# Performance work log

Hardware: AMD Instinct MI355X
Metric: run time of the kernel (lower is better)

## Reference

```python
import jax, jax.numpy as jnp
import numpy as np

ALPHA_LO = float(np.exp(-1.0 / 5.0))   # 0.8187
ALPHA_HI = float(np.exp(-1.0 / 25.0))  # 0.9608
BN_EPS = 1e-5

B, T, D_IN, H = 32, 2000, 512, 512


def setup_inputs() -> dict:
    key = jax.random.key(0)
    ks = jax.random.split(key, 5)
    x = jax.random.normal(ks[0], (B, T, D_IN), dtype=jnp.float32)
    W = jax.random.normal(ks[1], (H, D_IN), dtype=jnp.float32) / np.sqrt(D_IN)
    b = jax.random.normal(ks[2], (H,), dtype=jnp.float32) * 0.01
    alpha = jax.random.uniform(ks[3], (H,), dtype=jnp.float32,
                               minval=ALPHA_LO, maxval=ALPHA_HI)
    gamma = jnp.ones((H,), dtype=jnp.float32)
    beta = jnp.zeros((H,), dtype=jnp.float32)
    ut0 = jax.random.uniform(ks[4], (B, H), dtype=jnp.float32)
    return {"x": x, "W": W, "b": b, "alpha": alpha,
            "gamma": gamma, "beta": beta, "ut0": ut0}


def reference(x, W, b, alpha, gamma, beta, ut0):
    # Linear: [B,T,Din] @ [Din,H] + b
    Wx = jnp.einsum("btd,hd->bth", x, W) + b
    # BatchNorm1d (training forward): stats over flattened (B*T) dim
    flat = Wx.reshape(-1, Wx.shape[-1])
    mean = flat.mean(axis=0)
    var = flat.var(axis=0)  # biased, as torch BN uses for normalization
    Wx = ((flat - mean) * jax.lax.rsqrt(var + BN_EPS) * gamma + beta).reshape(Wx.shape)
    # Readout cell: leaky integration + softmax accumulation over time
    a = jnp.clip(alpha, ALPHA_LO, ALPHA_HI)

    def step(carry, wxt):
        ut, acc = carry
        ut = a * ut + (1.0 - a) * wxt          # [B,H]
        acc = acc + jax.nn.softmax(ut, axis=1)
        return (ut, acc), None

    wx_t = jnp.transpose(Wx, (1, 0, 2))  # [T,B,H]
    (_, out), _ = jax.lax.scan(step, (ut0, jnp.zeros_like(ut0)), wx_t)
    return out[:, None, :]  # [B,1,H]
```

## Files before the change

### kernel.cpp

```cpp
#include <hip/hip_runtime.h>
#include <hip/hip_bf16.h>
#include <stdint.h>


namespace {
constexpr int kB = 32;
constexpr int kT = 2000;
constexpr int kD = 512;
constexpr int kH = 512;
constexpr int kM = kB * kT;
constexpr int kL = 20;
constexpr int kC = kT / kL;
constexpr float kALo = 0.81873075307798182f;
constexpr float kAHi = 0.96078943915232320f;

typedef __bf16 bf16x4 __attribute__((ext_vector_type(4)));
typedef __bf16 bf16x8 __attribute__((ext_vector_type(8)));
typedef float floatx16 __attribute__((ext_vector_type(16)));

__device__ __forceinline__ float bf2f(unsigned short u) {
  return __builtin_bit_cast(float, (unsigned)u << 16);
}
__device__ __forceinline__ float clipa(float a) {
  return fminf(fmaxf(a, kALo), kAHi);
}
__device__ __forceinline__ float pow20(float a) {
  const float a2 = a * a, a4 = a2 * a2, a5 = a4 * a;
  const float a10 = a5 * a5;
  return a10 * a10;
}
__device__ __forceinline__ void gld_lds16(const void* g, void* l) {
  __builtin_amdgcn_global_load_lds(
      (const __attribute__((address_space(1))) uint32_t*)g,
      (__attribute__((address_space(3))) uint32_t*)(uintptr_t)l, 16, 0, 0);
}

__global__ __launch_bounds__(256) void wcvt_k(const float* __restrict__ W,
                                              __bf16* __restrict__ Wbf) {
  const int t = blockIdx.x * 256 + threadIdx.x;
  const float4 a0 = ((const float4*)W)[t * 2];
  const float4 a1 = ((const float4*)W)[t * 2 + 1];
  bf16x8 v;
  v[0] = (__bf16)a0.x; v[1] = (__bf16)a0.y; v[2] = (__bf16)a0.z; v[3] = (__bf16)a0.w;
  v[4] = (__bf16)a1.x; v[5] = (__bf16)a1.y; v[6] = (__bf16)a1.z; v[7] = (__bf16)a1.w;
  *(bf16x8*)(Wbf + (size_t)t * 8) = v;
}

__global__ __launch_bounds__(512, 2) void gemm_k(const float* __restrict__ X,
                                                 const __bf16* __restrict__ Wbf,
                                                 unsigned short* __restrict__ Wxb,
                                                 float* __restrict__ partial) {
  __shared__ __bf16 As[64][32];
  __shared__ __bf16 Bs[512][32];
  __shared__ float sred[2][kH];
  const int tid = threadIdx.x;
  const size_t row0 = (size_t)blockIdx.x * 64;
  const int w = tid >> 6, L = tid & 63;
  const int rt = w >> 2, ct0 = (w & 3) * 4;
  const int lhalf = L >> 5, l32 = L & 31;
  const int arow = tid >> 3, acol = (tid & 7) * 4;

  floatx16 acc[4] = {};
  const float* xbase = X + (row0 + arow) * kD + acol;
  float4 a_pre = *(const float4*)xbase;

#pragma unroll 1
  for (int s = 0; s < 16; ++s) {
    __syncthreads();
    bf16x4 av;
    av[0] = (__bf16)a_pre.x; av[1] = (__bf16)a_pre.y;
    av[2] = (__bf16)a_pre.z; av[3] = (__bf16)a_pre.w;
    *(bf16x4*)&As[arow][acol] = av;
    const int kk = s * 32;
#pragma unroll
    for (int j = 0; j < 4; ++j) {
      const int ci = j * 512 + w * 64 + L;
      const __bf16* src = Wbf + (size_t)(ci >> 2) * kD + kk + (ci & 3) * 8;
      gld_lds16(src, (char*)&Bs[0][0] + (size_t)ci * 16);
    }
    __syncthreads();
    if (s < 15) a_pre = *(const float4*)(xbase + (s + 1) * 32);
#pragma unroll
    for (int kh = 0; kh < 2; ++kh) {
      const bf16x8 af = *(const bf16x8*)&As[rt * 32 + l32][kh * 16 + lhalf * 8];
#pragma unroll
      for (int c = 0; c < 4; ++c) {
        const bf16x8 bfr = *(const bf16x8*)&Bs[(ct0 + c) * 32 + l32][kh * 16 + lhalf * 8];
        acc[c] = __builtin_amdgcn_mfma_f32_32x32x16_bf16(af, bfr, acc[c], 0, 0, 0);
      }
    }
  }

  __syncthreads();
  sred[0][tid] = 0.f;
  sred[1][tid] = 0.f;
  __syncthreads();
#pragma unroll
  for (int c = 0; c < 4; ++c) {
    float s = 0.f, q = 0.f;
#pragma unroll
    for (int r = 0; r < 16; ++r) {
      const float v = acc[c][r];
      s += v;
      q += v * v;
    }
    s += __shfl_xor(s, 32);
    q += __shfl_xor(q, 32);
    if (lhalf == 0) {
      atomicAdd(&sred[0][(ct0 + c) * 32 + l32], s);
      atomicAdd(&sred[1][(ct0 + c) * 32 + l32], q);
    }
  }
#pragma unroll
  for (int c = 0; c < 4; ++c) {
    const int col = (ct0 + c) * 32 + l32;
#pragma unroll
    for (int r = 0; r < 16; ++r) {
      const int row = rt * 32 + 4 * lhalf + (r & 3) + 8 * (r >> 2);
      const unsigned short u = __builtin_bit_cast(unsigned short, (__bf16)acc[c][r]);
      const unsigned un = __shfl_down((unsigned)u, 1);
      if ((l32 & 1) == 0)
        *(unsigned*)(Wxb + (row0 + row) * (size_t)kH + col) = (unsigned)u | (un << 16);
    }
  }
  __syncthreads();
  partial[(size_t)blockIdx.x * 1024 + tid] = sred[0][tid];
  partial[(size_t)blockIdx.x * 1024 + 512 + tid] = sred[1][tid];
}

__global__ __launch_bounds__(512) void red1_k(const float* __restrict__ partial,
                                              float* __restrict__ sums) {
  const int tid = threadIdx.x;
  const int r0 = blockIdx.x * 25;
  float s0 = 0.f, s1 = 0.f;
#pragma unroll 5
  for (int r = 0; r < 25; ++r) {
    s0 += partial[(size_t)(r0 + r) * 1024 + tid];
    s1 += partial[(size_t)(r0 + r) * 1024 + 512 + tid];
  }
  atomicAdd(&sums[tid], s0);
  atomicAdd(&sums[kH + tid], s1);
}

__global__ __launch_bounds__(512) void finalize_k(const float* __restrict__ sums,
                                                  const float* __restrict__ alpha,
                                                  const float* __restrict__ gamma,
                                                  const float* __restrict__ beta,
                                                  float* __restrict__ prm) {
  const int h = threadIdx.x;
  const float inv_n = 1.0f / (float)kM;
  const float mean = sums[h] * inv_n;
  const float var = sums[kH + h] * inv_n - mean * mean;
  const float sc = gamma[h] * rsqrtf(var + 1e-5f);
  const float sh = beta[h] - mean * sc;
  const float a = clipa(alpha[h]);
  prm[h] = sc;
  prm[kH + h] = sh;
  prm[2 * kH + h] = a;
  prm[3 * kH + h] = 1.0f - a;
  prm[4 * kH + h] = pow20(a);
}

__global__ __launch_bounds__(512) void agg_raw_k(const unsigned short* __restrict__ Wxb,
                                                 const float* __restrict__ alpha,
                                                 float* __restrict__ vbuf) {
  const int bc = blockIdx.x;
  const int b = bc / kC, c = bc % kC;
  const int h = threadIdx.x;
  const float a = clipa(alpha[h]);
  const float oma = 1.0f - a;
  const unsigned short* base = Wxb + ((size_t)b * kT + (size_t)c * kL) * kH + h;
  float v = 0.f;
#pragma unroll
  for (int i = 0; i < kL; ++i)
    v = a * v + oma * bf2f(base[(size_t)i * kH]);
  vbuf[(size_t)bc * kH + h] = v;
}

__global__ __launch_bounds__(512) void scan_k(const float* __restrict__ ut0,
                                              const float* __restrict__ alpha,
                                              const float* __restrict__ prm,
                                              float* __restrict__ vbuf) {
  const int b = blockIdx.x;
  const int h = threadIdx.x;
  const float a20 = pow20(clipa(alpha[h]));
  const float sc = prm[h];
  const float shc = prm[kH + h] * (1.0f - a20);
  float u = ut0[(size_t)b * kH + h];
  float vc[10];
#pragma unroll 1
  for (int cb = 0; cb < kC; cb += 10) {
#pragma unroll
    for (int j = 0; j < 10; ++j)
      vc[j] = vbuf[((size_t)b * kC + cb + j) * kH + h];
#pragma unroll
    for (int j = 0; j < 10; ++j) {
      vbuf[((size_t)b * kC + cb + j) * kH + h] = u;
      u = a20 * u + sc * vc[j] + shc;
    }
  }
}

__global__ __launch_bounds__(512) void soft_k(const unsigned short* __restrict__ Wxb,
                                              const float* __restrict__ prm,
                                              const float* __restrict__ ustart,
                                              float* __restrict__ accp) {
  __shared__ float part[kL][9];
  __shared__ float zinv[kL];
  const int bc = blockIdx.x;
  const int b = bc / kC, c = bc % kC;
  const int h = threadIdx.x;
  const int wv = h >> 6, lane = h & 63;
  const float sc = prm[h], sh = prm[kH + h];
  const float a = prm[2 * kH + h], oma = prm[3 * kH + h];
  float u = ustart[(size_t)bc * kH + h];
  const unsigned short* base = Wxb + ((size_t)b * kT + (size_t)c * kL) * kH + h;
  float e[kL];
#pragma unroll
  for (int i = 0; i < kL; ++i) {
    const float wvx = bf2f(base[(size_t)i * kH]) * sc + sh;
    u = a * u + oma * wvx;
    e[i] = __expf(u);
  }
#pragma unroll
  for (int i = 0; i < kL; ++i) {
    float s = e[i];
#pragma unroll
    for (int off = 32; off > 0; off >>= 1) s += __shfl_xor(s, off);
    if (lane == 0) part[i][wv] = s;
  }
  __syncthreads();
  if (h < kL) {
    float s = 0.f;
#pragma unroll
    for (int j = 0; j < 8; ++j) s += part[h][j];
    zinv[h] = 1.0f / s;
  }
  __syncthreads();
  float acc = 0.f;
#pragma unroll
  for (int i = 0; i < kL; ++i) acc += e[i] * zinv[i];
  accp[(size_t)bc * kH + h] = acc;
}

__global__ __launch_bounds__(512) void out_red_k(const float* __restrict__ accp,
                                                 float* __restrict__ out) {
  const int b = blockIdx.x;
  const int h = threadIdx.x;
  float s = 0.f;
#pragma unroll 4
  for (int c = 0; c < kC; ++c) s += accp[((size_t)b * kC + c) * kH + h];
  out[(size_t)b * kH + h] = s;
}

}

extern "C" void kernel_launch(void* const* d_in, const int* in_sizes, int n_in,
                              void* d_out, int out_size, void* d_ws, size_t ws_size,
                              hipStream_t stream) {
  const float* x = (const float*)d_in[0];
  const float* Wm = (const float*)d_in[1];
  const float* alpha = (const float*)d_in[3];
  const float* gamma = (const float*)d_in[4];
  const float* beta = (const float*)d_in[5];
  const float* ut0 = (const float*)d_in[6];
  float* out = (float*)d_out;

  float* wsp = (float*)d_ws;
  float* vbuf = wsp;
  float* accp = vbuf + (size_t)kB * kC * kH;
  float* partial = accp + (size_t)kB * kC * kH;
  float* sums = partial + (size_t)1000 * 1024;
  float* prm = sums + 2 * kH;
  __bf16* Wbf = (__bf16*)(prm + 5 * kH);
  unsigned short* Wxb = (unsigned short*)(Wbf + (size_t)kH * kD);

  hipMemsetAsync(sums, 0, 2 * kH * sizeof(float), stream);
  wcvt_k<<<128, 256, 0, stream>>>(Wm, Wbf);
  gemm_k<<<kM / 64, 512, 0, stream>>>(x, Wbf, Wxb, partial);
  agg_raw_k<<<kB * kC, 512, 0, stream>>>(Wxb, alpha, vbuf);
  red1_k<<<40, 512, 0, stream>>>(partial, sums);
  finalize_k<<<1, 512, 0, stream>>>(sums, alpha, gamma, beta, prm);
  scan_k<<<kB, 512, 0, stream>>>(ut0, alpha, prm, vbuf);
  soft_k<<<kB * kC, 512, 0, stream>>>(Wxb, prm, vbuf, accp);
  out_red_k<<<kB, 512, 0, stream>>>(accp, out);
}
```

Measured before the change: 317.8 us.

## Double-buffer GEMM tiles, vectorize scan kernels, drop atomics and memset

The GEMM now double-buffers its A and B tiles. The next step's W DMA and X loads are issued before the current MFMAs, and the fragments are stored in an MFMA-friendly layout, so there is one barrier per k-step instead of two. The BN statistics reduction is rewritten as a two-level deterministic reduce, which removes the atomics and the memset launch. agg, soft and out_red are vectorized so each thread handles 8 or 4 channels with wide loads, using smaller blocks and more blocks for out_red. The cost is more LDS in the GEMM, which may lower occupancy, and more registers in soft_k.

```diff
diff --git a/kernel.cpp b/kernel.cpp
--- a/kernel.cpp
+++ b/kernel.cpp
@@ -14,7 +14,6 @@
 constexpr float kALo = 0.81873075307798182f;
 constexpr float kAHi = 0.96078943915232320f;
 
-typedef __bf16 bf16x4 __attribute__((ext_vector_type(4)));
 typedef __bf16 bf16x8 __attribute__((ext_vector_type(8)));
 typedef float floatx16 __attribute__((ext_vector_type(16)));
 
@@ -50,48 +49,71 @@
                                                  const __bf16* __restrict__ Wbf,
                                                  unsigned short* __restrict__ Wxb,
                                                  float* __restrict__ partial) {
-  __shared__ __bf16 As[64][32];
-  __shared__ __bf16 Bs[512][32];
+  __shared__ __align__(16) char AsB[2][4 * 1024];
+  __shared__ __align__(16) char BsB[2][32 * 1024];
   __shared__ float sred[2][kH];
   const int tid = threadIdx.x;
   const size_t row0 = (size_t)blockIdx.x * 64;
   const int w = tid >> 6, L = tid & 63;
   const int rt = w >> 2, ct0 = (w & 3) * 4;
   const int lhalf = L >> 5, l32 = L & 31;
-  const int arow = tid >> 3, acol = (tid & 7) * 4;
+  const int am = tid >> 2, akq = tid & 3;
+  const int a_off = ((am >> 5) * 2 + (akq >> 1)) * 1024 + ((akq & 1) * 32 + (am & 31)) * 16;
+  const float* xptr = X + (row0 + am) * kD + akq * 8;
 
   floatx16 acc[4] = {};
-  const float* xbase = X + (row0 + arow) * kD + acol;
-  float4 a_pre = *(const float4*)xbase;
+  float4 ap0, ap1;
+
+  auto loadA = [&](int s) {
+    if (tid < 256) {
+      const float4* p = (const float4*)(xptr + s * 32);
+      ap0 = p[0]; ap1 = p[1];
+    }
+  };
+  auto storeA = [&](int buf) {
+    if (tid < 256) {
+      bf16x8 v;
+      v[0] = (__bf16)ap0.x; v[1] = (__bf16)ap0.y; v[2] = (__bf16)ap0.z; v[3] = (__bf16)ap0.w;
+      v[4] = (__bf16)ap1.x; v[5] = (__bf16)ap1.y; v[6] = (__bf16)ap1.z; v[7] = (__bf16)ap1.w;
+      *(bf16x8*)(AsB[buf] + a_off) = v;
+    }
+  };
+  auto dmaB = [&](int s, int buf) {
+#pragma unroll
+    for (int j = 0; j < 4; ++j) {
+      const int q = w * 4 + j;
+      const int n = (q >> 1) * 32 + l32;
+      const int k = s * 32 + (q & 1) * 16 + lhalf * 8;
+      gld_lds16(Wbf + (size_t)n * kD + k, BsB[buf] + q * 1024);
+    }
+  };
+
+  loadA(0);
+  dmaB(0, 0);
+  storeA(0);
+  __syncthreads();
 
 #pragma unroll 1
   for (int s = 0; s < 16; ++s) {
-    __syncthreads();
-    bf16x4 av;
-    av[0] = (__bf16)a_pre.x; av[1] = (__bf16)a_pre.y;
-    av[2] = (__bf16)a_pre.z; av[3] = (__bf16)a_pre.w;
-    *(bf16x4*)&As[arow][acol] = av;
-    const int kk = s * 32;
-#pragma unroll
-    for (int j = 0; j < 4; ++j) {
-      const int ci = j * 512 + w * 64 + L;
-      const __bf16* src = Wbf + (size_t)(ci >> 2) * kD + kk + (ci & 3) * 8;
-      gld_lds16(src, (char*)&Bs[0][0] + (size_t)ci * 16);
-    }
-    __syncthreads();
-    if (s < 15) a_pre = *(const float4*)(xbase + (s + 1) * 32);
+    const int cur = s & 1, nxt = cur ^ 1;
+    if (s < 15) {
+      dmaB(s + 1, nxt);
+      loadA(s + 1);
+    }
 #pragma unroll
     for (int kh = 0; kh < 2; ++kh) {
-      const bf16x8 af = *(const bf16x8*)&As[rt * 32 + l32][kh * 16 + lhalf * 8];
+      const bf16x8 af = *(const bf16x8*)(AsB[cur] + (rt * 2 + kh) * 1024 + L * 16);
 #pragma unroll
       for (int c = 0; c < 4; ++c) {
-        const bf16x8 bfr = *(const bf16x8*)&Bs[(ct0 + c) * 32 + l32][kh * 16 + lhalf * 8];
+        const bf16x8 bfr =
+            *(const bf16x8*)(BsB[cur] + ((ct0 + c) * 2 + kh) * 1024 + L * 16);
         acc[c] = __builtin_amdgcn_mfma_f32_32x32x16_bf16(af, bfr, acc[c], 0, 0, 0);
       }
     }
-  }
-
-  __syncthreads();
+    if (s < 15) storeA(nxt);
+    __syncthreads();
+  }
+
   sred[0][tid] = 0.f;
   sred[1][tid] = 0.f;
   __syncthreads();
@@ -129,7 +151,7 @@
 }
 
 __global__ __launch_bounds__(512) void red1_k(const float* __restrict__ partial,
-                                              float* __restrict__ sums) {
+                                              float* __restrict__ partial2) {
   const int tid = threadIdx.x;
   const int r0 = blockIdx.x * 25;
   float s0 = 0.f, s1 = 0.f;
@@ -138,19 +160,25 @@
     s0 += partial[(size_t)(r0 + r) * 1024 + tid];
     s1 += partial[(size_t)(r0 + r) * 1024 + 512 + tid];
   }
-  atomicAdd(&sums[tid], s0);
-  atomicAdd(&sums[kH + tid], s1);
-}
-
-__global__ __launch_bounds__(512) void finalize_k(const float* __restrict__ sums,
+  partial2[(size_t)blockIdx.x * 1024 + tid] = s0;
+  partial2[(size_t)blockIdx.x * 1024 + 512 + tid] = s1;
+}
+
+__global__ __launch_bounds__(512) void finalize_k(const float* __restrict__ partial2,
                                                   const float* __restrict__ alpha,
                                                   const float* __restrict__ gamma,
                                                   const float* __restrict__ beta,
                                                   float* __restrict__ prm) {
   const int h = threadIdx.x;
+  float s0 = 0.f, s1 = 0.f;
+#pragma unroll 8
+  for (int r = 0; r < 40; ++r) {
+    s0 += partial2[(size_t)r * 1024 + h];
+    s1 += partial2[(size_t)r * 1024 + 512 + h];
+  }
   const float inv_n = 1.0f / (float)kM;
-  const float mean = sums[h] * inv_n;
-  const float var = sums[kH + h] * inv_n - mean * mean;
+  const float mean = s0 * inv_n;
+  const float var = s1 * inv_n - mean * mean;
   const float sc = gamma[h] * rsqrtf(var + 1e-5f);
   const float sh = beta[h] - mean * sc;
   const float a = clipa(alpha[h]);
@@ -161,20 +189,37 @@
   prm[4 * kH + h] = pow20(a);
 }
 
-__global__ __launch_bounds__(512) void agg_raw_k(const unsigned short* __restrict__ Wxb,
-                                                 const float* __restrict__ alpha,
-                                                 float* __restrict__ vbuf) {
-  const int bc = blockIdx.x;
-  const int b = bc / kC, c = bc % kC;
-  const int h = threadIdx.x;
-  const float a = clipa(alpha[h]);
-  const float oma = 1.0f - a;
-  const unsigned short* base = Wxb + ((size_t)b * kT + (size_t)c * kL) * kH + h;
-  float v = 0.f;
-#pragma unroll
-  for (int i = 0; i < kL; ++i)
-    v = a * v + oma * bf2f(base[(size_t)i * kH]);
-  vbuf[(size_t)bc * kH + h] = v;
+__global__ __launch_bounds__(256) void agg_k(const unsigned short* __restrict__ Wxb,
+                                             const float* __restrict__ alpha,
+                                             float* __restrict__ vbuf) {
+  const int g = blockIdx.x;
+  const int b = g / (kC / 4), cg = g % (kC / 4);
+  const int wv = threadIdx.x >> 6, lane = threadIdx.x & 63;
+  const int c = cg * 4 + wv;
+  const int h0 = lane * 8;
+  float a[8], v[8];
+  const float4 av0 = *(const float4*)(alpha + h0);
+  const float4 av1 = *(const float4*)(alpha + h0 + 4);
+  a[0] = av0.x; a[1] = av0.y; a[2] = av0.z; a[3] = av0.w;
+  a[4] = av1.x; a[5] = av1.y; a[6] = av1.z; a[7] = av1.w;
+#pragma unroll
+  for (int j = 0; j < 8; ++j) { a[j] = clipa(a[j]); v[j] = 0.f; }
+  const unsigned short* base = Wxb + ((size_t)b * kT + (size_t)c * kL) * kH + h0;
+#pragma unroll
+  for (int i = 0; i < kL; ++i) {
+    const uint4 p = *(const uint4*)(base + (size_t)i * kH);
+    const unsigned pw[4] = {p.x, p.y, p.z, p.w};
+#pragma unroll
+    for (int d = 0; d < 4; ++d) {
+      const float w0 = bf2f((unsigned short)(pw[d] & 0xffff));
+      const float w1 = bf2f((unsigned short)(pw[d] >> 16));
+      v[2 * d] = a[2 * d] * v[2 * d] + (1.f - a[2 * d]) * w0;
+      v[2 * d + 1] = a[2 * d + 1] * v[2 * d + 1] + (1.f - a[2 * d + 1]) * w1;
+    }
+  }
+  float* dst = vbuf + ((size_t)b * kC + c) * kH + h0;
+  *(float4*)dst = make_float4(v[0], v[1], v[2], v[3]);
+  *(float4*)(dst + 4) = make_float4(v[4], v[5], v[6], v[7]);
 }
 
 __global__ __launch_bounds__(512) void scan_k(const float* __restrict__ ut0,
@@ -201,54 +246,61 @@
   }
 }
 
-__global__ __launch_bounds__(512) void soft_k(const unsigned short* __restrict__ Wxb,
+__global__ __launch_bounds__(128) void soft_k(const unsigned short* __restrict__ Wxb,
                                               const float* __restrict__ prm,
                                               const float* __restrict__ ustart,
                                               float* __restrict__ accp) {
-  __shared__ float part[kL][9];
+  __shared__ float part[kL][2];
   __shared__ float zinv[kL];
   const int bc = blockIdx.x;
   const int b = bc / kC, c = bc % kC;
-  const int h = threadIdx.x;
-  const int wv = h >> 6, lane = h & 63;
-  const float sc = prm[h], sh = prm[kH + h];
-  const float a = prm[2 * kH + h], oma = prm[3 * kH + h];
-  float u = ustart[(size_t)bc * kH + h];
-  const unsigned short* base = Wxb + ((size_t)b * kT + (size_t)c * kL) * kH + h;
-  float e[kL];
+  const int t = threadIdx.x;
+  const int wv = t >> 6, lane = t & 63;
+  const int h0 = t * 4;
+  const float4 sc = *(const float4*)(prm + h0);
+  const float4 sh = *(const float4*)(prm + kH + h0);
+  const float4 aa = *(const float4*)(prm + 2 * kH + h0);
+  const float4 om = *(const float4*)(prm + 3 * kH + h0);
+  float4 u = *(const float4*)(ustart + (size_t)bc * kH + h0);
+  const unsigned short* base = Wxb + ((size_t)b * kT + (size_t)c * kL) * kH + h0;
+  float e[kL][4];
 #pragma unroll
   for (int i = 0; i < kL; ++i) {
-    const float wvx = bf2f(base[(size_t)i * kH]) * sc + sh;
-    u = a * u + oma * wvx;
-    e[i] = __expf(u);
-  }
-#pragma unroll
-  for (int i = 0; i < kL; ++i) {
-    float s = e[i];
+    const uint2 p = *(const uint2*)(base + (size_t)i * kH);
+    const float w0 = bf2f((unsigned short)(p.x & 0xffff)) * sc.x + sh.x;
+    const float w1 = bf2f((unsigned short)(p.x >> 16)) * sc.y + sh.y;
+    const float w2 = bf2f((unsigned short)(p.y & 0xffff)) * sc.z + sh.z;
+    const float w3 = bf2f((unsigned short)(p.y >> 16)) * sc.w + sh.w;
+    u.x = aa.x * u.x + om.x * w0;
+    u.y = aa.y * u.y + om.y * w1;
+    u.z = aa.z * u.z + om.z * w2;
+    u.w = aa.w * u.w + om.w * w3;
+    e[i][0] = __expf(u.x); e[i][1] = __expf(u.y);
+    e[i][2] = __expf(u.z); e[i][3] = __expf(u.w);
+    float s = (e[i][0] + e[i][1]) + (e[i][2] + e[i][3]);
 #pragma unroll
     for (int off = 32; off > 0; off >>= 1) s += __shfl_xor(s, off);
     if (lane == 0) part[i][wv] = s;
   }
   __syncthreads();
-  if (h < kL) {
-    float s = 0.f;
-#pragma unroll
-    for (int j = 0; j < 8; ++j) s += part[h][j];
-    zinv[h] = 1.0f / s;
-  }
-  __syncthreads();
-  float acc = 0.f;
-#pragma unroll
-  for (int i = 0; i < kL; ++i) acc += e[i] * zinv[i];
-  accp[(size_t)bc * kH + h] = acc;
-}
-
-__global__ __launch_bounds__(512) void out_red_k(const float* __restrict__ accp,
+  if (t < kL) zinv[t] = 1.0f / (part[t][0] + part[t][1]);
+  __syncthreads();
+  float4 o = make_float4(0.f, 0.f, 0.f, 0.f);
+#pragma unroll
+  for (int i = 0; i < kL; ++i) {
+    const float z = zinv[i];
+    o.x += e[i][0] * z; o.y += e[i][1] * z;
+    o.z += e[i][2] * z; o.w += e[i][3] * z;
+  }
+  *(float4*)(accp + (size_t)bc * kH + h0) = o;
+}
+
+__global__ __launch_bounds__(128) void out_red_k(const float* __restrict__ accp,
                                                  float* __restrict__ out) {
-  const int b = blockIdx.x;
-  const int h = threadIdx.x;
+  const int b = blockIdx.x >> 2, q = blockIdx.x & 3;
+  const int h = q * 128 + threadIdx.x;
   float s = 0.f;
-#pragma unroll 4
+#pragma unroll 5
   for (int c = 0; c < kC; ++c) s += accp[((size_t)b * kC + c) * kH + h];
   out[(size_t)b * kH + h] = s;
 }
@@ -270,18 +322,17 @@
   float* vbuf = wsp;
   float* accp = vbuf + (size_t)kB * kC * kH;
   float* partial = accp + (size_t)kB * kC * kH;
-  float* sums = partial + (size_t)1000 * 1024;
-  float* prm = sums + 2 * kH;
+  float* partial2 = partial + (size_t)1000 * 1024;
+  float* prm = partial2 + (size_t)40 * 1024;
   __bf16* Wbf = (__bf16*)(prm + 5 * kH);
   unsigned short* Wxb = (unsigned short*)(Wbf + (size_t)kH * kD);
 
-  hipMemsetAsync(sums, 0, 2 * kH * sizeof(float), stream);
   wcvt_k<<<128, 256, 0, stream>>>(Wm, Wbf);
   gemm_k<<<kM / 64, 512, 0, stream>>>(x, Wbf, Wxb, partial);
-  agg_raw_k<<<kB * kC, 512, 0, stream>>>(Wxb, alpha, vbuf);
-  red1_k<<<40, 512, 0, stream>>>(partial, sums);
-  finalize_k<<<1, 512, 0, stream>>>(sums, alpha, gamma, beta, prm);
+  red1_k<<<40, 512, 0, stream>>>(partial, partial2);
+  agg_k<<<kB * (kC / 4), 256, 0, stream>>>(Wxb, alpha, vbuf);
+  finalize_k<<<1, 512, 0, stream>>>(partial2, alpha, gamma, beta, prm);
   scan_k<<<kB, 512, 0, stream>>>(ut0, alpha, prm, vbuf);
-  soft_k<<<kB * kC, 512, 0, stream>>>(Wxb, prm, vbuf, accp);
-  out_red_k<<<kB, 512, 0, stream>>>(accp, out);
-}
+  soft_k<<<kB * kC, 128, 0, stream>>>(Wxb, prm, vbuf, accp);
+  out_red_k<<<kB * 4, 128, 0, stream>>>(accp, out);
+}
```

Result: slower. 336.9 us (+6.0%).
